# Kernel tuning notes

Measured on AMD Instinct MI355X. Metric: run time of the kernel, lower is better.

The kernel has to match this reference:

```python
import jax, jax.numpy as jnp
import numpy as np


def _skip_plan(T, skip_size):
    """Static per-step plan replicating Python list indexing h_i_skips[i - skip_size].

    Returns (slots, use_zero): slot k means 'use h from k+1 steps ago' in the
    rolling buffer (buf[0] == h_{i-1}); use_zero==1 means the skip input is a
    zero init vector.
    """
    slots = np.zeros(T, np.int32)
    use_zero = np.zeros(T, np.float32)
    for i in range(T):
        if i < skip_size:
            # negative Python index: element 2*i of [skip_size zeros] + appended h's
            if 2 * i < skip_size:
                use_zero[i] = 1.0
            else:
                # h_j with j = 2*i - skip_size  ->  lag = i - j = skip_size - i
                slots[i] = (skip_size - i) - 1
        else:
            if i - skip_size < skip_size:
                use_zero[i] = 1.0  # one of the zero inits
            else:
                slots[i] = 2 * skip_size - 1  # h_{i - 2*skip_size}
    return jnp.asarray(slots), jnp.asarray(use_zero)


def setup_inputs() -> dict:
    key = jax.random.key(0)
    ks = jax.random.split(key, 7)
    B, T, X, H = 64, 512, 256, 1024
    s = 1.0 / float(np.sqrt(H))  # PyTorch GRUCell init scale
    x = jax.random.normal(ks[0], (B, T, X), jnp.float32)
    W_ih = jax.random.uniform(ks[1], (3 * H, X), jnp.float32, -s, s)
    W_hh = jax.random.uniform(ks[2], (3 * H, H), jnp.float32, -s, s)
    b_ih = jax.random.uniform(ks[3], (3 * H,), jnp.float32, -s, s)
    b_hh = jax.random.uniform(ks[4], (3 * H,), jnp.float32, -s, s)
    w1 = jax.random.randint(ks[5], (T,), 0, 2, jnp.int32)
    w2_rand = jax.random.randint(ks[6], (T,), 0, 2, jnp.int32)
    w2 = jnp.where(w1 == 0, 1, w2_rand)  # original: W_2 = 1 if W_1 == 0
    return {"x": x, "W_ih": W_ih, "W_hh": W_hh, "b_ih": b_ih, "b_hh": b_hh,
            "w1": w1, "w2": w2, "skip_size": 5}


def reference(x, W_ih, W_hh, b_ih, b_hh, w1, w2, skip_size):
    B, T, X = x.shape
    H = W_hh.shape[1]
    slots, use_zero = _skip_plan(T, int(skip_size))
    # Batch all input projections up-front: [T, B, 3H]
    xi = jnp.einsum('btx,gx->tbg', x, W_ih) + b_ih
    L = 2 * int(skip_size)
    buf0 = jnp.zeros((L, B, H), x.dtype)  # buf[k] = h_{i-1-k}
    w1f = w1.astype(x.dtype)
    w2f = w2.astype(x.dtype)

    def step(buf, xs):
        xi_t, a, b, slot, uz = xs
        h_orig = buf[0]
        h_skip = jax.lax.dynamic_index_in_dim(buf, slot, 0, keepdims=False)
        h = h_orig * a + h_skip * b * (1.0 - uz)
        hh = h @ W_hh.T + b_hh
        xr, xz, xn = jnp.split(xi_t, 3, axis=-1)
        hr, hz, hn = jnp.split(hh, 3, axis=-1)
        r = jax.nn.sigmoid(xr + hr)
        z = jax.nn.sigmoid(xz + hz)
        n = jnp.tanh(xn + r * hn)
        h_new = (1.0 - z) * n + z * h
        buf = jnp.concatenate([h_new[None], buf[:-1]], axis=0)
        return buf, None

    buf, _ = jax.lax.scan(step, buf0, (xi, w1f, w2f, slots, use_zero))
    # h_i_original + h_i_skip, and chunk(repeat) makes them identical
    return 2.0 * buf[0]
```

## Files before the change

### kernel.cpp

```cpp
#include <hip/hip_runtime.h>
#include <hip/hip_bf16.h>
#include <type_traits>

typedef short bf16x8 __attribute__((ext_vector_type(8)));
typedef short bf16x4 __attribute__((ext_vector_type(4)));
typedef float f32x4  __attribute__((ext_vector_type(4)));
typedef unsigned long long u64;

#define B_   64
#define T_   512
#define XD_  256
#define H_   1024
#define NWG  256

#define OFF_WCAT  0UL
#define SZ_WCAT   (3072UL*1280*2)
#define OFF_XB    (OFF_WCAT + SZ_WCAT)
#define SZ_XB     ((unsigned long)T_*B_*XD_*2)
#define OFF_HBF16 (OFF_XB + SZ_XB)
#define SZ_HBF16  (2UL*B_*H_*2)
#define OFF_PLAN  (OFF_HBF16 + SZ_HBF16)
#define SZ_PLAN   (4096UL)
#define OFF_CNT   (OFF_PLAN + SZ_PLAN)

__device__ __forceinline__ float sigm_(float x) { return 1.f / (1.f + __expf(-x)); }
__device__ __forceinline__ float tanh_(float x) { return 1.f - 2.f / (__expf(2.f * x) + 1.f); }
__device__ __forceinline__ short bf16_of(float f) {
    __hip_bfloat16 h = __float2bfloat16(f);
    return *reinterpret_cast<short*>(&h);
}
__device__ __forceinline__ float f_of_bf16(short s) {
    union { unsigned u; float f; } c;
    c.u = ((unsigned)(unsigned short)s) << 16;
    return c.f;
}

__global__ void prep_wcat(const float* __restrict__ W_ih, const float* __restrict__ W_hh,
                          short* __restrict__ Wcat) {
    const int j = blockIdx.x;
    for (int k = threadIdx.x; k < 1280; k += 256) {
        float v = (k < XD_) ? W_ih[j * XD_ + k] : W_hh[j * H_ + (k - XD_)];
        Wcat[(long)j * 1280 + k] = bf16_of(v);
    }
}

__global__ void prep_xb(const float* __restrict__ x, short* __restrict__ xb) {
    const long total = (long)T_ * B_ * XD_;
    for (long i = (long)blockIdx.x * blockDim.x + threadIdx.x; i < total;
         i += (long)gridDim.x * blockDim.x) {
        int t   = (int)(i >> 14);
        int rem = (int)(i & 16383);
        int b   = rem >> 8;
        int k   = rem & 255;
        xb[i] = bf16_of(x[((long)(b * T_ + t)) * XD_ + k]);
    }
}

__global__ void prep_plan(const int* __restrict__ w1, const int* __restrict__ w2,
                          const int* __restrict__ ssp, int* __restrict__ plang) {
    int t = threadIdx.x;
    if (t > T_) return;
    if (t == T_) { plang[t] = (1 << 2); return; }
    int ss = ssp[0];
    int a = w1[t] & 1;
    int uz = 0, slot = 0;
    if (t < ss)            { if (2 * t < ss) uz = 1; else slot = ss - t - 1; }
    else if (t - ss < ss)  { uz = 1; }
    else                   { slot = 2 * ss - 1; }
    int bet = uz ? 0 : (w2[t] & 1);
    plang[t] = a | (bet << 1) | ((slot + 1) << 2);
}

__global__ void prep_zero(short* __restrict__ hbf16, unsigned* __restrict__ cnt) {
    int i = blockIdx.x * blockDim.x + threadIdx.x;
    if (i < B_ * H_) hbf16[i] = 0;
    if (i < 1024) cnt[i] = 0u;
}

__global__ __launch_bounds__(256, 1) void persist_kernel(
    const short* __restrict__ Wcat, const short* __restrict__ xb,
    const float* __restrict__ b_ih, const float* __restrict__ b_hh,
    short* __restrict__ hbf16, const int* __restrict__ plang,
    unsigned* __restrict__ cnt, float* __restrict__ out) {

    __shared__ short Wlds[48 * 1280];
    __shared__ float red[3][3][64][4];
    __shared__ short ringl[16][16][20];
    __shared__ float hbls[2][16][20];
    __shared__ int   planl[T_ + 1];

    const int tid = threadIdx.x;
    const int w   = tid >> 6;
    const int l   = tid & 63;
    const int l15 = l & 15;
    const int lhi = l >> 4;
    const int wg  = blockIdx.x;
    const int c0  = (wg >> 2) << 4;
    const int m0  = (wg & 3) << 4;
    const int grp = wg & 7;
    const int jc0 = c0 + lhi * 4;

    for (int j = tid; j < 48 * 160; j += 256) {
        int r    = j / 160;
        int cbyt = (j - r * 160) * 16;
        int g    = r >> 4, i = r & 15;
        bf16x8 v = *(const bf16x8*)(Wcat + (long)(g * H_ + c0 + i) * 1280 + (cbyt >> 1));
        *(bf16x8*)((char*)Wlds + r * 2560 + (cbyt ^ (i << 4))) = v;
    }
    for (int j = tid; j <= T_; j += 256) planl[j] = plang[j];
    for (int j = tid; j < 2 * 16 * 20; j += 256) ((float*)hbls)[j] = 0.f;

    const f32x4 brc = *(const f32x4*)&b_ih[jc0]          + *(const f32x4*)&b_hh[jc0];
    const f32x4 bzc = *(const f32x4*)&b_ih[H_ + jc0]     + *(const f32x4*)&b_hh[H_ + jc0];
    const f32x4 bin = *(const f32x4*)&b_ih[2 * H_ + jc0];
    const f32x4 bhn = *(const f32x4*)&b_hh[2 * H_ + jc0];
    __syncthreads();

    const int swz = l15 << 4;
    auto arow = [&](int g, int kb) -> bf16x8 {
        return *(const bf16x8*)((const char*)Wlds + (g * 16 + l15) * 2560 + (kb ^ swz));
    };

    f32x4 accX[3];
    auto xgemm = [&](int t) {
        accX[0] = accX[1] = accX[2] = (f32x4){0.f, 0.f, 0.f, 0.f};
        const short* xp = xb + ((long)t * B_ + m0 + l15) * XD_ + lhi * 8;
        #pragma unroll
        for (int it = 0; it < 8; ++it) {
            bf16x8 bfrag = *(const bf16x8*)(xp + it * 32);
            const int kb = (it * 32 + lhi * 8) * 2;
            accX[0] = __builtin_amdgcn_mfma_f32_16x16x32_bf16(arow(0, kb), bfrag, accX[0], 0, 0, 0);
            accX[1] = __builtin_amdgcn_mfma_f32_16x16x32_bf16(arow(1, kb), bfrag, accX[1], 0, 0, 0);
            accX[2] = __builtin_amdgcn_mfma_f32_16x16x32_bf16(arow(2, kb), bfrag, accX[2], 0, 0, 0);
        }
    };

    if (w == 0) xgemm(0);

    int cur = 0;
    for (int t = 0; t < T_; ++t) {
        if (w > 0) {
            f32x4 accH[3] = {{0.f,0.f,0.f,0.f},{0.f,0.f,0.f,0.f},{0.f,0.f,0.f,0.f}};
            const short* hb16 = hbf16 + (long)cur * (B_ * H_);
            auto hgemm = [&](auto ITC, int hk0) {
                constexpr int IT = decltype(ITC)::value;
                const short* sp = hb16 + (m0 + l15) * H_ + hk0 + lhi * 8;
                const u64*   hp = (const u64*)sp;
                u64 lo[IT], hi[IT];
                #pragma unroll
                for (int it = 0; it < IT; ++it) {
                    lo[it] = __hip_atomic_load(hp + it * 8,     __ATOMIC_RELAXED, __HIP_MEMORY_SCOPE_SYSTEM);
                    hi[it] = __hip_atomic_load(hp + it * 8 + 1, __ATOMIC_RELAXED, __HIP_MEMORY_SCOPE_SYSTEM);
                }
                #pragma unroll
                for (int it = 0; it < IT; ++it) {
                    union { u64 q[2]; bf16x8 v; } uu;
                    uu.q[0] = lo[it]; uu.q[1] = hi[it];
                    const int kb = (256 + hk0 + it * 32 + lhi * 8) * 2;
                    accH[0] = __builtin_amdgcn_mfma_f32_16x16x32_bf16(arow(0, kb), uu.v, accH[0], 0, 0, 0);
                    accH[1] = __builtin_amdgcn_mfma_f32_16x16x32_bf16(arow(1, kb), uu.v, accH[1], 0, 0, 0);
                    accH[2] = __builtin_amdgcn_mfma_f32_16x16x32_bf16(arow(2, kb), uu.v, accH[2], 0, 0, 0);
                }
            };
            if      (w == 1) hgemm(std::integral_constant<int, 11>{}, 0);
            else if (w == 2) hgemm(std::integral_constant<int, 11>{}, 352);
            else             hgemm(std::integral_constant<int, 10>{}, 704);
            #pragma unroll
            for (int g = 0; g < 3; ++g)
                *(f32x4*)&red[g][w - 1][l][0] = accH[g];
        }
        __syncthreads();

        if (w == 0) {
            f32x4 Hr = {0.f,0.f,0.f,0.f}, Hz = {0.f,0.f,0.f,0.f}, Hn = {0.f,0.f,0.f,0.f};
            #pragma unroll
            for (int s = 0; s < 3; ++s) {
                Hr += *(const f32x4*)&red[0][s][l][0];
                Hz += *(const f32x4*)&red[1][s][l][0];
                Hn += *(const f32x4*)&red[2][s][l][0];
            }
            const int   p   = planl[t + 1];
            const float al  = (float)(p & 1);
            const float bet = (float)((p >> 1) & 1);
            const int   lg  = p >> 2;

            const f32x4 hb = *(const f32x4*)&hbls[cur][l15][lhi * 4];
            f32x4 hn;
            #pragma unroll
            for (int r = 0; r < 4; ++r) {
                float rg = sigm_(accX[0][r] + Hr[r] + brc[r]);
                float zg = sigm_(accX[1][r] + Hz[r] + bzc[r]);
                float ng = tanh_(accX[2][r] + bin[r] + rg * (Hn[r] + bhn[r]));
                hn[r] = (1.f - zg) * ng + zg * hb[r];
            }
            union { short s[4]; u64 q; } pk;
            #pragma unroll
            for (int r = 0; r < 4; ++r) pk.s[r] = bf16_of(hn[r]);
            *(bf16x4*)&ringl[t & 15][l15][lhi * 4] = *(bf16x4*)pk.s;
            const bf16x4 old4 = *(const bf16x4*)&ringl[(t + 1 - lg) & 15][l15][lhi * 4];
            f32x4 hbn;
            #pragma unroll
            for (int r = 0; r < 4; ++r)
                hbn[r] = al * hn[r] + bet * f_of_bf16(old4[r]);
            *(f32x4*)&hbls[cur ^ 1][l15][lhi * 4] = hbn;
            #pragma unroll
            for (int r = 0; r < 4; ++r) pk.s[r] = bf16_of(hbn[r]);
            u64* pub = (u64*)(hbf16 + (long)(cur ^ 1) * (B_ * H_) + (m0 + l15) * H_ + jc0);
            __hip_atomic_store(pub, pk.q, __ATOMIC_RELAXED, __HIP_MEMORY_SCOPE_SYSTEM);

            if (t == T_ - 1) {
                f32x4 o = hn; o[0] *= 2.f; o[1] *= 2.f; o[2] *= 2.f; o[3] *= 2.f;
                *(f32x4*)&out[(long)(m0 + l15) * H_ + jc0] = o;
            }

            if (t + 1 < T_) {
                if (tid == 0) {
                    asm volatile("s_waitcnt vmcnt(0)" ::: "memory");
                    unsigned old = __hip_atomic_fetch_add(&cnt[grp * 32], 1u,
                                        __ATOMIC_RELAXED, __HIP_MEMORY_SCOPE_AGENT);
                    if (old == 32u * (unsigned)(t + 1) - 1u)
                        __hip_atomic_fetch_add(&cnt[512], 1u,
                                        __ATOMIC_RELAXED, __HIP_MEMORY_SCOPE_AGENT);
                }
                xgemm(t + 1);
                if (tid == 0) {
                    const unsigned tgt = 8u * (unsigned)(t + 1);
                    while (__hip_atomic_load(&cnt[512], __ATOMIC_RELAXED,
                                             __HIP_MEMORY_SCOPE_AGENT) < tgt)
                        __builtin_amdgcn_s_sleep(2);
                }
            }
        }
        __syncthreads();
        cur ^= 1;
    }
}

extern "C" void kernel_launch(void* const* d_in, const int* in_sizes, int n_in,
                              void* d_out, int out_size, void* d_ws, size_t ws_size,
                              hipStream_t stream) {
    const float* x    = (const float*)d_in[0];
    const float* W_ih = (const float*)d_in[1];
    const float* W_hh = (const float*)d_in[2];
    const float* b_ih = (const float*)d_in[3];
    const float* b_hh = (const float*)d_in[4];
    const int*   w1   = (const int*)d_in[5];
    const int*   w2   = (const int*)d_in[6];
    const int*   ssp  = (const int*)d_in[7];
    float* out = (float*)d_out;

    char* ws = (char*)d_ws;
    short*    Wcat  = (short*)(ws + OFF_WCAT);
    short*    xbuf  = (short*)(ws + OFF_XB);
    short*    hbf16 = (short*)(ws + OFF_HBF16);
    int*      plang = (int*)(ws + OFF_PLAN);
    unsigned* cnt   = (unsigned*)(ws + OFF_CNT);

    prep_wcat<<<3072, 256, 0, stream>>>(W_ih, W_hh, Wcat);
    prep_xb<<<8192, 256, 0, stream>>>(x, xbuf);
    prep_plan<<<1, 1024, 0, stream>>>(w1, w2, ssp, plang);
    prep_zero<<<256, 256, 0, stream>>>(hbf16, cnt);

    persist_kernel<<<NWG, 256, 0, stream>>>(Wcat, xbuf, b_ih, b_hh,
                                            hbf16, plang, cnt, out);
}
```

Baseline: 2.508 ms.

## Replace global atomic counter barrier with per-domain step flags polled by consumer waves

Replaces the grid-wide two-level atomic counter barrier with per-workgroup step flags grouped by batch slice, since each workgroup only needs h from the 64 workgroups sharing its rows. Consumer waves poll those flags directly with a vectorized system-coherent load, and the second per-step __syncthreads is removed. To make that safe, the reduction buffer is double-buffered. The h loads and stores use raw dwordx4/dwordx2 instructions with sc0 sc1 instead of split 64-bit atomics. This narrows synchronization to the real data dependency and cuts barrier latency on the critical serial path. The cost is more polling traffic and reliance on hand-written memory-ordering asm.

New measurement: 2.688 ms. 1.07x slower.

```diff
diff --git a/kernel.cpp b/kernel.cpp
--- a/kernel.cpp
+++ b/kernel.cpp
@@ -5,6 +5,7 @@
 typedef short bf16x8 __attribute__((ext_vector_type(8)));
 typedef short bf16x4 __attribute__((ext_vector_type(4)));
 typedef float f32x4  __attribute__((ext_vector_type(4)));
+typedef int   i32x4  __attribute__((ext_vector_type(4)));
 typedef unsigned long long u64;
 
 #define B_   64
@@ -21,7 +22,7 @@
 #define SZ_HBF16  (2UL*B_*H_*2)
 #define OFF_PLAN  (OFF_HBF16 + SZ_HBF16)
 #define SZ_PLAN   (4096UL)
-#define OFF_CNT   (OFF_PLAN + SZ_PLAN)
+#define OFF_FLAG  (OFF_PLAN + SZ_PLAN)
 
 __device__ __forceinline__ float sigm_(float x) { return 1.f / (1.f + __expf(-x)); }
 __device__ __forceinline__ float tanh_(float x) { return 1.f - 2.f / (__expf(2.f * x) + 1.f); }
@@ -71,20 +72,20 @@
     plang[t] = a | (bet << 1) | ((slot + 1) << 2);
 }
 
-__global__ void prep_zero(short* __restrict__ hbf16, unsigned* __restrict__ cnt) {
+__global__ void prep_zero(short* __restrict__ hbf16, int* __restrict__ flags) {
     int i = blockIdx.x * blockDim.x + threadIdx.x;
     if (i < B_ * H_) hbf16[i] = 0;
-    if (i < 1024) cnt[i] = 0u;
+    if (i < 1024) flags[i] = 0;
 }
 
 __global__ __launch_bounds__(256, 1) void persist_kernel(
     const short* __restrict__ Wcat, const short* __restrict__ xb,
     const float* __restrict__ b_ih, const float* __restrict__ b_hh,
     short* __restrict__ hbf16, const int* __restrict__ plang,
-    unsigned* __restrict__ cnt, float* __restrict__ out) {
+    int* __restrict__ flags, float* __restrict__ out) {
 
     __shared__ short Wlds[48 * 1280];
-    __shared__ float red[3][3][64][4];
+    __shared__ float red[2][3][3][64][4];
     __shared__ short ringl[16][16][20];
     __shared__ float hbls[2][16][20];
     __shared__ int   planl[T_ + 1];
@@ -97,7 +98,8 @@
     const int wg  = blockIdx.x;
     const int c0  = (wg >> 2) << 4;
     const int m0  = (wg & 3) << 4;
-    const int grp = wg & 7;
+    const int dom = wg & 3;
+    const int idx = wg >> 2;
     const int jc0 = c0 + lhi * 4;
 
     for (int j = tid; j < 48 * 160; j += 256) {
@@ -134,28 +136,41 @@
             accX[2] = __builtin_amdgcn_mfma_f32_16x16x32_bf16(arow(2, kb), bfrag, accX[2], 0, 0, 0);
         }
     };
-
     if (w == 0) xgemm(0);
 
-    int cur = 0;
     for (int t = 0; t < T_; ++t) {
+        const int cur = t & 1, nxt = cur ^ 1, par = t & 1;
+
         if (w > 0) {
+            if (t > 0) {
+                const int* fa = flags + dom * 64 + ((l & 15) << 2);
+                while (true) {
+                    i32x4 f;
+                    asm volatile("global_load_dwordx4 %0, %1, off sc0 sc1\n\t"
+                                 "s_waitcnt vmcnt(0)"
+                                 : "=&v"(f) : "v"(fa) : "memory");
+                    int m01 = f[0] < f[1] ? f[0] : f[1];
+                    int m23 = f[2] < f[3] ? f[2] : f[3];
+                    int mn  = m01 < m23 ? m01 : m23;
+                    if (__all((l < 16) ? (mn >= t) : 1)) break;
+                }
+                __builtin_amdgcn_sched_barrier(0);
+            }
+
             f32x4 accH[3] = {{0.f,0.f,0.f,0.f},{0.f,0.f,0.f,0.f},{0.f,0.f,0.f,0.f}};
-            const short* hb16 = hbf16 + (long)cur * (B_ * H_);
             auto hgemm = [&](auto ITC, int hk0) {
                 constexpr int IT = decltype(ITC)::value;
-                const short* sp = hb16 + (m0 + l15) * H_ + hk0 + lhi * 8;
-                const u64*   hp = (const u64*)sp;
-                u64 lo[IT], hi[IT];
+                const short* hp = hbf16 + (long)cur * (B_ * H_) + (m0 + l15) * H_ + hk0 + lhi * 8;
+                i32x4 hv[IT];
+                #pragma unroll
+                for (int it = 0; it < IT; ++it)
+                    asm volatile("global_load_dwordx4 %0, %1, off sc0 sc1"
+                                 : "=&v"(hv[it]) : "v"(hp + it * 32));
+                asm volatile("s_waitcnt vmcnt(0)" ::: "memory");
+                __builtin_amdgcn_sched_barrier(0);
                 #pragma unroll
                 for (int it = 0; it < IT; ++it) {
-                    lo[it] = __hip_atomic_load(hp + it * 8,     __ATOMIC_RELAXED, __HIP_MEMORY_SCOPE_SYSTEM);
-                    hi[it] = __hip_atomic_load(hp + it * 8 + 1, __ATOMIC_RELAXED, __HIP_MEMORY_SCOPE_SYSTEM);
-                }
-                #pragma unroll
-                for (int it = 0; it < IT; ++it) {
-                    union { u64 q[2]; bf16x8 v; } uu;
-                    uu.q[0] = lo[it]; uu.q[1] = hi[it];
+                    union { i32x4 q; bf16x8 v; } uu; uu.q = hv[it];
                     const int kb = (256 + hk0 + it * 32 + lhi * 8) * 2;
                     accH[0] = __builtin_amdgcn_mfma_f32_16x16x32_bf16(arow(0, kb), uu.v, accH[0], 0, 0, 0);
                     accH[1] = __builtin_amdgcn_mfma_f32_16x16x32_bf16(arow(1, kb), uu.v, accH[1], 0, 0, 0);
@@ -167,7 +182,7 @@
             else             hgemm(std::integral_constant<int, 10>{}, 704);
             #pragma unroll
             for (int g = 0; g < 3; ++g)
-                *(f32x4*)&red[g][w - 1][l][0] = accH[g];
+                *(f32x4*)&red[par][g][w - 1][l][0] = accH[g];
         }
         __syncthreads();
 
@@ -175,9 +190,9 @@
             f32x4 Hr = {0.f,0.f,0.f,0.f}, Hz = {0.f,0.f,0.f,0.f}, Hn = {0.f,0.f,0.f,0.f};
             #pragma unroll
             for (int s = 0; s < 3; ++s) {
-                Hr += *(const f32x4*)&red[0][s][l][0];
-                Hz += *(const f32x4*)&red[1][s][l][0];
-                Hn += *(const f32x4*)&red[2][s][l][0];
+                Hr += *(const f32x4*)&red[par][0][s][l][0];
+                Hz += *(const f32x4*)&red[par][1][s][l][0];
+                Hn += *(const f32x4*)&red[par][2][s][l][0];
             }
             const int   p   = planl[t + 1];
             const float al  = (float)(p & 1);
@@ -202,37 +217,28 @@
             #pragma unroll
             for (int r = 0; r < 4; ++r)
                 hbn[r] = al * hn[r] + bet * f_of_bf16(old4[r]);
-            *(f32x4*)&hbls[cur ^ 1][l15][lhi * 4] = hbn;
+            *(f32x4*)&hbls[nxt][l15][lhi * 4] = hbn;
+
             #pragma unroll
             for (int r = 0; r < 4; ++r) pk.s[r] = bf16_of(hbn[r]);
-            u64* pub = (u64*)(hbf16 + (long)(cur ^ 1) * (B_ * H_) + (m0 + l15) * H_ + jc0);
-            __hip_atomic_store(pub, pk.q, __ATOMIC_RELAXED, __HIP_MEMORY_SCOPE_SYSTEM);
+            short* pub = hbf16 + (long)nxt * (B_ * H_) + (m0 + l15) * H_ + jc0;
+            asm volatile("global_store_dwordx2 %0, %1, off sc0 sc1"
+                         :: "v"(pub), "v"(pk.q) : "memory");
 
             if (t == T_ - 1) {
                 f32x4 o = hn; o[0] *= 2.f; o[1] *= 2.f; o[2] *= 2.f; o[3] *= 2.f;
                 *(f32x4*)&out[(long)(m0 + l15) * H_ + jc0] = o;
-            }
-
-            if (t + 1 < T_) {
+            } else {
+                asm volatile("s_waitcnt vmcnt(0)" ::: "memory");
                 if (tid == 0) {
-                    asm volatile("s_waitcnt vmcnt(0)" ::: "memory");
-                    unsigned old = __hip_atomic_fetch_add(&cnt[grp * 32], 1u,
-                                        __ATOMIC_RELAXED, __HIP_MEMORY_SCOPE_AGENT);
-                    if (old == 32u * (unsigned)(t + 1) - 1u)
-                        __hip_atomic_fetch_add(&cnt[512], 1u,
-                                        __ATOMIC_RELAXED, __HIP_MEMORY_SCOPE_AGENT);
+                    int* fp = flags + dom * 64 + idx;
+                    int fv = t + 1;
+                    asm volatile("global_store_dword %0, %1, off sc0 sc1"
+                                 :: "v"(fp), "v"(fv) : "memory");
                 }
                 xgemm(t + 1);
-                if (tid == 0) {
-                    const unsigned tgt = 8u * (unsigned)(t + 1);
-                    while (__hip_atomic_load(&cnt[512], __ATOMIC_RELAXED,
-                                             __HIP_MEMORY_SCOPE_AGENT) < tgt)
-                        __builtin_amdgcn_s_sleep(2);
-                }
             }
         }
-        __syncthreads();
-        cur ^= 1;
     }
 }
 
@@ -250,17 +256,17 @@
     float* out = (float*)d_out;
 
     char* ws = (char*)d_ws;
-    short*    Wcat  = (short*)(ws + OFF_WCAT);
-    short*    xbuf  = (short*)(ws + OFF_XB);
-    short*    hbf16 = (short*)(ws + OFF_HBF16);
-    int*      plang = (int*)(ws + OFF_PLAN);
-    unsigned* cnt   = (unsigned*)(ws + OFF_CNT);
+    short* Wcat  = (short*)(ws + OFF_WCAT);
+    short* xbuf  = (short*)(ws + OFF_XB);
+    short* hbf16 = (short*)(ws + OFF_HBF16);
+    int*   plang = (int*)(ws + OFF_PLAN);
+    int*   flags = (int*)(ws + OFF_FLAG);
 
     prep_wcat<<<3072, 256, 0, stream>>>(W_ih, W_hh, Wcat);
     prep_xb<<<8192, 256, 0, stream>>>(x, xbuf);
     prep_plan<<<1, 1024, 0, stream>>>(w1, w2, ssp, plang);
-    prep_zero<<<256, 256, 0, stream>>>(hbf16, cnt);
+    prep_zero<<<256, 256, 0, stream>>>(hbf16, flags);
 
     persist_kernel<<<NWG, 256, 0, stream>>>(Wcat, xbuf, b_ih, b_hh,
-                                            hbf16, plang, cnt, out);
-}
+                                            hbf16, plang, flags, out);
+}
```
